# Kernel optimization log

Hardware: AMD Instinct MI355X
Metric: run time of the kernel (lower is better)

Reference implementation:

```python
import jax, jax.numpy as jnp
import numpy as np

HEADS = 16
ROPE_BASE = 10000.0


def _rope(x):
    # x: [b, h, n, d]. lucidrains partial rotary: RotaryEmbedding(head_dim//2)
    # rotates only the first rot_dim = d//2 channels, interleaved-pair style.
    d = x.shape[-1]
    rot = d // 2
    inv_freq = 1.0 / (ROPE_BASE ** (jnp.arange(0, rot, 2, dtype=jnp.float32) / rot))  # [rot//2]
    pos = jnp.arange(x.shape[2], dtype=jnp.float32)
    freqs = pos[:, None] * inv_freq[None, :]                  # [n, rot//2]
    cos, sin = jnp.cos(freqs), jnp.sin(freqs)
    xr, xp = x[..., :rot], x[..., rot:]
    x1, x2 = xr[..., 0::2], xr[..., 1::2]                     # interleaved pairs
    o1 = x1 * cos - x2 * sin
    o2 = x2 * cos + x1 * sin
    xr_out = jnp.stack([o1, o2], axis=-1).reshape(xr.shape)   # re-interleave
    return jnp.concatenate([xr_out, xp], axis=-1)


def setup_inputs() -> dict:
    key = jax.random.key(0)
    k0, k1 = jax.random.split(key)
    B, N, D = 2, 2048, 2048
    x = jax.random.normal(k0, (B, N, D), dtype=jnp.float32)
    W_qkv = jax.random.normal(k1, (3 * D, D), dtype=jnp.float32) * (D ** -0.5)
    b_qkv = jnp.zeros((3 * D,), dtype=jnp.float32)
    return {"x": x, "W_qkv": W_qkv, "b_qkv": b_qkv}


def reference(x, W_qkv, b_qkv):
    B, N, D = x.shape
    H = HEADS
    hd = D // H
    qkv = x @ W_qkv.T + b_qkv                                  # [b, n, 3d]
    q, k, v = jnp.split(qkv, 3, axis=-1)
    to_heads = lambda t: t.reshape(B, N, H, hd).transpose(0, 2, 1, 3)  # b h n d
    q, k, v = to_heads(q), to_heads(k), to_heads(v)
    q, k = _rope(q), _rope(k)
    scale = 1.0 / np.sqrt(hd)
    scores = jnp.einsum('bhnd,bhmd->bhnm', q, k) * scale
    causal = jnp.tril(jnp.ones((N, N), dtype=bool))
    scores = jnp.where(causal, scores, -jnp.inf)
    attn = jax.nn.softmax(scores, axis=-1)
    y = jnp.einsum('bhnm,bhmd->bhnd', attn, v)
    return y.transpose(0, 2, 1, 3).reshape(B, N, D)
```

## Files before the change

### kernel.cpp

```cpp
#include <hip/hip_runtime.h>
#include <hip/hip_bf16.h>
#include <math.h>

typedef unsigned short u16;
typedef unsigned int u32;
typedef __attribute__((ext_vector_type(8))) short bf16x8;
typedef __attribute__((ext_vector_type(4))) float f32x4;

#define B_ 2
#define N_ 2048
#define D_ 2048
#define H_ 16
#define HD 128
#define GK 2048

__device__ __forceinline__ u16 f2bf(float f) {
  u32 u = __float_as_uint(f);
  u = (u + 0x7fffu + ((u >> 16) & 1u)) >> 16;
  return (u16)u;
}

__device__ __forceinline__ u32 cvtpk(float lo, float hi) {
  u32 r;
  asm("v_cvt_pk_bf16_f32 %0, %1, %2" : "=v"(r) : "v"(lo), "v"(hi));
  return r;
}

__device__ __forceinline__ void gload_lds16(const void* g, void* l) {
  __builtin_amdgcn_global_load_lds(
      (const __attribute__((address_space(1))) u32*)g,
      (__attribute__((address_space(3))) u32*)l, 16, 0, 0);
}

__global__ __launch_bounds__(256) void cvt_kernel(const float* __restrict__ in,
                                                  u16* __restrict__ out, int n4) {
  int i = blockIdx.x * blockDim.x + threadIdx.x;
  int st = gridDim.x * blockDim.x;
  for (; i < n4; i += st) {
    float4 v = ((const float4*)in)[i];
    ushort4 o;
    o.x = f2bf(v.x); o.y = f2bf(v.y); o.z = f2bf(v.z); o.w = f2bf(v.w);
    ((ushort4*)out)[i] = o;
  }
}

__global__ __launch_bounds__(256) void rope_tbl_kernel(float* __restrict__ tbl) {
  int i = blockIdx.x * blockDim.x + threadIdx.x;
  if (i >= N_ * 32) return;
  int pos = i >> 5, p = i & 31;
  double inv = pow(10000.0, -(double)p / 32.0);
  double a = (double)pos * inv;
  tbl[2 * i]     = (float)cos(a);
  tbl[2 * i + 1] = (float)sin(a);
}

__global__ __launch_bounds__(512, 2) void qkv_gemm_kernel(
    const u16* __restrict__ X, const u16* __restrict__ W,
    const float* __restrict__ bias, const float* __restrict__ tbl,
    u16* __restrict__ Qo, u16* __restrict__ Ko, u16* __restrict__ Vo) {
  __shared__ char smem[114688];
  const int tid = threadIdx.x;
  const int lane = tid & 63;
  const int w = tid >> 6;
  const int wm = w >> 2, wn = w & 3;
  const int l15 = lane & 15, l4 = lane >> 4;

  const int bid = blockIdx.x;
  const int wg = (bid & 7) * 64 + (bid >> 3);
  const int n0 = (wg & 31) * 192;
  const int m0 = (wg >> 5) * 256;

  f32x4 acc[8][3];
#pragma unroll
  for (int fm = 0; fm < 8; ++fm)
#pragma unroll
    for (int fn = 0; fn < 3; ++fn)
#pragma unroll
      for (int q = 0; q < 4; ++q) acc[fm][fn][q] = 0.f;

  auto stageA = [&](int cb, int half, int k0) {
    char* dst = smem + cb * 57344 + half * 16384;
    const u16* src = X + (size_t)(m0 + half * 128) * GK + k0;
#pragma unroll
    for (int p = 0; p < 2; ++p) {
      int o = (w * 2 + p) * 1024 + lane * 16;
      int lo = o ^ (((o >> 7) & 7) << 4);
      gload_lds16(src + (size_t)(lo >> 7) * GK + ((lo & 127) >> 1),
                  dst + (w * 2 + p) * 1024);
    }
  };
  auto stageB = [&](int cb, int chunk, int k0) {
    char* dst = smem + cb * 57344 + 32768 + chunk * 8192;
    const u16* src = W + (size_t)(n0 + chunk * 64) * GK + k0;
    int o = w * 1024 + lane * 16;
    int lo = o ^ (((o >> 7) & 7) << 4);
    gload_lds16(src + (size_t)(lo >> 7) * GK + ((lo & 127) >> 1), dst + w * 1024);
  };

  const int NK = GK / 64;

  stageA(0, 0, 0); stageA(0, 1, 0);
  stageB(0, 0, 0); stageB(0, 1, 0); stageB(0, 2, 0);
  stageA(1, 0, 64); stageA(1, 1, 64);
  asm volatile("s_waitcnt vmcnt(4)" ::: "memory");
  __builtin_amdgcn_s_barrier();

  auto segment = [&](int T, int cb) {
    const char* Ab = smem + cb * 57344 + wm * 16384;
    const char* Bb = smem + cb * 57344 + 32768;
    const int kn1 = (T + 1) * 64, kn2 = (T + 2) * 64;
    bf16x8 a0[8], a1[8], b0[3], b1[3];

#pragma unroll
    for (int fm = 0; fm < 8; ++fm) {
      int r = fm * 16 + l15;
      a0[fm] = *(const bf16x8*)(Ab + ((r * 128 + l4 * 16) ^ ((r & 7) << 4)));
    }
#pragma unroll
    for (int fn = 0; fn < 3; ++fn) {
      int r = wn * 48 + fn * 16 + l15;
      b0[fn] = *(const bf16x8*)(Bb + ((r * 128 + l4 * 16) ^ ((r & 7) << 4)));
    }
    if (T + 1 < NK) { stageB(cb ^ 1, 0, kn1); stageB(cb ^ 1, 1, kn1); }
    __builtin_amdgcn_s_barrier();
    __builtin_amdgcn_s_setprio(1);
#pragma unroll
    for (int fm = 0; fm < 4; ++fm)
#pragma unroll
      for (int fn = 0; fn < 3; ++fn)
        acc[fm][fn] = __builtin_amdgcn_mfma_f32_16x16x32_bf16(a0[fm], b0[fn], acc[fm][fn], 0, 0, 0);
    __builtin_amdgcn_s_setprio(0);
    __builtin_amdgcn_s_barrier();

#pragma unroll
    for (int fm = 0; fm < 8; ++fm) {
      int r = fm * 16 + l15;
      a1[fm] = *(const bf16x8*)(Ab + ((r * 128 + 64 + l4 * 16) ^ ((r & 7) << 4)));
    }
#pragma unroll
    for (int fn = 0; fn < 3; ++fn) {
      int r = wn * 48 + fn * 16 + l15;
      b1[fn] = *(const bf16x8*)(Bb + ((r * 128 + 64 + l4 * 16) ^ ((r & 7) << 4)));
    }
    if (T + 1 < NK) stageB(cb ^ 1, 2, kn1);
    __builtin_amdgcn_s_barrier();
    __builtin_amdgcn_s_setprio(1);
#pragma unroll
    for (int fm = 4; fm < 8; ++fm)
#pragma unroll
      for (int fn = 0; fn < 3; ++fn)
        acc[fm][fn] = __builtin_amdgcn_mfma_f32_16x16x32_bf16(a0[fm], b0[fn], acc[fm][fn], 0, 0, 0);
    __builtin_amdgcn_s_setprio(0);
    __builtin_amdgcn_s_barrier();

    asm volatile("" ::: "memory");
    if (T + 2 < NK) stageA(cb, 0, kn2);
    __builtin_amdgcn_s_barrier();
    __builtin_amdgcn_s_setprio(1);
#pragma unroll
    for (int fm = 0; fm < 4; ++fm)
#pragma unroll
      for (int fn = 0; fn < 3; ++fn)
        acc[fm][fn] = __builtin_amdgcn_mfma_f32_16x16x32_bf16(a1[fm], b1[fn], acc[fm][fn], 0, 0, 0);
    __builtin_amdgcn_s_setprio(0);
    __builtin_amdgcn_s_barrier();

    asm volatile("" ::: "memory");
    if (T + 2 < NK) {
      stageA(cb, 1, kn2);
      asm volatile("s_waitcnt vmcnt(4)" ::: "memory");
    } else {
      asm volatile("s_waitcnt vmcnt(0)" ::: "memory");
    }
    __builtin_amdgcn_s_barrier();
    __builtin_amdgcn_s_setprio(1);
#pragma unroll
    for (int fm = 4; fm < 8; ++fm)
#pragma unroll
      for (int fn = 0; fn < 3; ++fn)
        acc[fm][fn] = __builtin_amdgcn_mfma_f32_16x16x32_bf16(a1[fm], b1[fn], acc[fm][fn], 0, 0, 0);
    __builtin_amdgcn_s_setprio(0);
    __builtin_amdgcn_s_barrier();
  };

  for (int T = 0; T < NK; T += 2) { segment(T, 0); segment(T + 1, 1); }

  const float QSCALE = 0.08838834764831845f;
#pragma unroll
  for (int fn = 0; fn < 3; ++fn) {
    int gn = n0 + wn * 48 + fn * 16 + l15;
    float bv = bias[gn];
    int sec = gn >> 11;
    int wi = gn & 2047;
    int h = wi >> 7;
    int d = wi & 127;
    u16* dstbase = (sec == 0) ? Qo : (sec == 1) ? Ko : Vo;
    float mulf = (sec == 0) ? QSCALE : 1.f;
    bool doRope = (sec < 2) && (d < 64);
    int pidx = d >> 1;
    bool odd = (d & 1) != 0;
#pragma unroll
    for (int fm = 0; fm < 8; ++fm) {
#pragma unroll
      for (int j = 0; j < 4; ++j) {
        int gm = m0 + wm * 128 + fm * 16 + l4 * 4 + j;
        int bb = gm >> 11;
        int pos = gm & 2047;
        float v = acc[fm][fn][j] + bv;
        float pr = __shfl_xor(v, 1);
        float ov = v;
        if (doRope) {
          float2 cs = ((const float2*)tbl)[pos * 32 + pidx];
          ov = odd ? (v * cs.x + pr * cs.y) : (v * cs.x - pr * cs.y);
        }
        dstbase[(size_t)((bb * H_ + h) * N_ + pos) * HD + d] = f2bf(ov * mulf);
      }
    }
  }
}

__global__ __launch_bounds__(256, 2) void flash_kernel(
    const u16* __restrict__ Q, const u16* __restrict__ K, const u16* __restrict__ V,
    float* __restrict__ Out) {
  __shared__ char smem[69632];

  const int tid = threadIdx.x, lane = tid & 63, w = tid >> 6;
  const int l15 = lane & 15, l4 = lane >> 4;

  const int bid = blockIdx.x;
  const int xcd = bid & 7, slot = bid >> 3;
  const int bh = xcd * 4 + (slot >> 4);
  const int x = 15 - (slot & 15);
  const int bb = bh >> 4, h = bh & 15;
  const size_t base = (size_t)bh * (N_ * HD);
  const int q0 = x * 128;
  const int nt = 2 * x + 2;

  bf16x8 qf[2][4];
#pragma unroll
  for (int g = 0; g < 2; ++g) {
    const u16* qp = Q + base + (size_t)(q0 + w * 32 + g * 16 + l15) * HD + l4 * 8;
#pragma unroll
    for (int kf = 0; kf < 4; ++kf) qf[g][kf] = *(const bf16x8*)(qp + kf * 32);
  }

  float m_r[2] = {-1e30f, -1e30f}, l_r[2] = {0.f, 0.f};
  f32x4 accO[2][8];
#pragma unroll
  for (int g = 0; g < 2; ++g)
#pragma unroll
    for (int df = 0; df < 8; ++df)
#pragma unroll
      for (int q = 0; q < 4; ++q) accO[g][df][q] = 0.f;

  auto stageK = [&](int buf, int t0) {
    const u16* kb = K + base + (size_t)t0 * HD;
    char* kt = smem + buf * 16384;
#pragma unroll
    for (int i = 0; i < 4; ++i) {
      int c = w * 4 + i;
      int o = c * 1024 + lane * 16;
      int lo = o ^ (((o >> 8) & 7) << 4);
      gload_lds16(kb + (lo >> 1), kt + c * 1024);
    }
  };
  auto loadV = [&](int t0, bf16x8* vr) {
    const u16* vp = V + base + (size_t)(t0 + lane) * HD + w * 32;
#pragma unroll
    for (int i = 0; i < 4; ++i) vr[i] = *(const bf16x8*)(vp + i * 8);
  };
  auto writeV = [&](int buf, const bf16x8* vr) {
    u16* vt = (u16*)(smem + 32768 + buf * 18432);
#pragma unroll
    for (int i = 0; i < 4; ++i)
#pragma unroll
      for (int jj = 0; jj < 8; ++jj)
        vt[(w * 32 + i * 8 + jj) * 72 + lane] = (u16)vr[i][jj];
  };

  const int src0 = l15 + 32 * (l4 & 1);
  const int src1 = src0 + 16;
  const int half = l4 >> 1;
  union U8 { u32 u[4]; bf16x8 v; };

  bf16x8 vreg[4];
  stageK(0, 0);
  loadV(0, vreg);
  writeV(0, vreg);
  __syncthreads();

  for (int t = 0; t < nt; ++t) {
    const int cur = t & 1;
    const int t0 = t * 64;
    const bool pre = (t + 1 < nt);
    if (pre) { stageK(cur ^ 1, t0 + 64); loadV(t0 + 64, vreg); }

    const char* kt = smem + cur * 16384;
    const u16* vt = (const u16*)(smem + 32768 + cur * 18432);

    f32x4 s[2][4];
#pragma unroll
    for (int cf = 0; cf < 4; ++cf) {
#pragma unroll
      for (int q = 0; q < 4; ++q) { s[0][cf][q] = 0.f; s[1][cf][q] = 0.f; }
      int row = cf * 16 + l15;
      int sw = (row & 7) << 4;
#pragma unroll
      for (int kf = 0; kf < 4; ++kf) {
        int off = (row * 256 + kf * 64 + l4 * 16) ^ sw;
        bf16x8 kfrag = *(const bf16x8*)(kt + off);
        s[0][cf] = __builtin_amdgcn_mfma_f32_16x16x32_bf16(kfrag, qf[0][kf], s[0][cf], 0, 0, 0);
        s[1][cf] = __builtin_amdgcn_mfma_f32_16x16x32_bf16(kfrag, qf[1][kf], s[1][cf], 0, 0, 0);
      }
    }

    u32 pk[2][4][2];
#pragma unroll
    for (int g = 0; g < 2; ++g) {
      const int qbase = q0 + w * 32 + g * 16;
      if (t0 + 63 > qbase) {
        const int qg = qbase + l15;
#pragma unroll
        for (int cf = 0; cf < 4; ++cf)
#pragma unroll
          for (int j = 0; j < 4; ++j) {
            int kvg = t0 + cf * 16 + l4 * 4 + j;
            if (kvg > qg) s[g][cf][j] = -1e30f;
          }
      }
      float pmax = s[g][0][0];
#pragma unroll
      for (int cf = 0; cf < 4; ++cf)
#pragma unroll
        for (int j = 0; j < 4; ++j) pmax = fmaxf(pmax, s[g][cf][j]);
      pmax = fmaxf(pmax, __shfl_xor(pmax, 16));
      pmax = fmaxf(pmax, __shfl_xor(pmax, 32));

      if (!__all(pmax <= m_r[g] + 8.f)) {
        float mn = fmaxf(m_r[g], pmax);
        float rs = __expf(m_r[g] - mn);
        m_r[g] = mn;
        l_r[g] *= rs;
#pragma unroll
        for (int df = 0; df < 8; ++df)
#pragma unroll
          for (int j = 0; j < 4; ++j) accO[g][df][j] *= rs;
      }

      float ps = 0.f;
#pragma unroll
      for (int cf = 0; cf < 4; ++cf) {
        float p0 = __expf(s[g][cf][0] - m_r[g]);
        float p1 = __expf(s[g][cf][1] - m_r[g]);
        float p2 = __expf(s[g][cf][2] - m_r[g]);
        float p3 = __expf(s[g][cf][3] - m_r[g]);
        ps += (p0 + p1) + (p2 + p3);
        pk[g][cf][0] = cvtpk(p0, p1);
        pk[g][cf][1] = cvtpk(p2, p3);
      }
      ps += __shfl_xor(ps, 16);
      ps += __shfl_xor(ps, 32);
      l_r[g] += ps;
    }

#pragma unroll
    for (int c = 0; c < 2; ++c) {
      const int c2 = 2 * c;
      U8 pu[2];
#pragma unroll
      for (int g = 0; g < 2; ++g) {
        u32 a0 = (u32)__shfl((int)pk[g][c2][0], src0);
        u32 b0 = (u32)__shfl((int)pk[g][c2 + 1][0], src0);
        u32 a1 = (u32)__shfl((int)pk[g][c2][1], src0);
        u32 b1 = (u32)__shfl((int)pk[g][c2 + 1][1], src0);
        u32 a2 = (u32)__shfl((int)pk[g][c2][0], src1);
        u32 b2 = (u32)__shfl((int)pk[g][c2 + 1][0], src1);
        u32 a3 = (u32)__shfl((int)pk[g][c2][1], src1);
        u32 b3 = (u32)__shfl((int)pk[g][c2 + 1][1], src1);
        pu[g].u[0] = half ? b0 : a0;
        pu[g].u[1] = half ? b1 : a1;
        pu[g].u[2] = half ? b2 : a2;
        pu[g].u[3] = half ? b3 : a3;
      }
#pragma unroll
      for (int df = 0; df < 8; ++df) {
        bf16x8 vf = *(const bf16x8*)(vt + (df * 16 + l15) * 72 + c * 32 + l4 * 8);
        accO[0][df] = __builtin_amdgcn_mfma_f32_16x16x32_bf16(vf, pu[0].v, accO[0][df], 0, 0, 0);
        accO[1][df] = __builtin_amdgcn_mfma_f32_16x16x32_bf16(vf, pu[1].v, accO[1][df], 0, 0, 0);
      }
    }

    if (pre) writeV(cur ^ 1, vreg);
    __syncthreads();
  }

  float* Obuf = (float*)(smem + w * 8448);
  const int l31 = lane & 31;
#pragma unroll
  for (int g = 0; g < 2; ++g) {
    float inv = 1.f / l_r[g];
#pragma unroll
    for (int df = 0; df < 8; ++df) {
      f32x4 v = accO[g][df];
#pragma unroll
      for (int j = 0; j < 4; ++j) v[j] *= inv;
      *(f32x4*)&Obuf[l15 * 132 + df * 16 + l4 * 4] = v;
    }
#pragma unroll
    for (int p = 0; p < 8; ++p) {
      int row = p * 2 + (lane >> 5);
      f32x4 v = *(const f32x4*)&Obuf[row * 132 + l31 * 4];
      int qg = q0 + w * 32 + g * 16 + row;
      *(f32x4*)&Out[(size_t)(bb * N_ + qg) * D_ + h * HD + l31 * 4] = v;
    }
  }
}

extern "C" void kernel_launch(void* const* d_in, const int* in_sizes, int n_in,
                              void* d_out, int out_size, void* d_ws, size_t ws_size,
                              hipStream_t stream) {
  const float* x  = (const float*)d_in[0];
  const float* Wq = (const float*)d_in[1];
  const float* bq = (const float*)d_in[2];
  float* out = (float*)d_out;
  char* ws = (char*)d_ws;

  u16* Qb  = (u16*)(ws);
  u16* Kb  = (u16*)(ws + 16777216);
  u16* Vb  = (u16*)(ws + 2 * 16777216);
  u16* Xb  = (u16*)(ws + 3 * 16777216);
  u16* Wb  = (u16*)(ws + 4 * 16777216);
  float* tbl = (float*)(ws + 4 * 16777216 + 25165824);

  cvt_kernel<<<2048, 256, 0, stream>>>(x, Xb, (B_ * N_ * D_) / 4);
  cvt_kernel<<<2048, 256, 0, stream>>>(Wq, Wb, (3 * D_ * D_) / 4);
  rope_tbl_kernel<<<(N_ * 32 + 255) / 256, 256, 0, stream>>>(tbl);
  qkv_gemm_kernel<<<512, 512, 0, stream>>>(Xb, Wb, bq, tbl, Qb, Kb, Vb);
  flash_kernel<<<512, 256, 0, stream>>>(Qb, Kb, Vb, out);
}
```

Before: 255.4 us.

## Triple-buffer A tiles and load fragments just-in-time in QKV GEMM

Restructures the QKV GEMM main loop so the A operand uses three LDS buffers and B uses two, with separate rotation. Each quarter-step now loads only the 4 A and 3 B fragments it needs, instead of preloading 8+8 A and 3+3 B, which cuts register pressure. Staging address arithmetic is hoisted out of the loop. LDS use grows from 112KB to 144KB, which may limit the 2-blocks-per-CU launch bound and changes where the LDS reads sit relative to the barriers.

```diff
diff --git a/kernel.cpp b/kernel.cpp
--- a/kernel.cpp
+++ b/kernel.cpp
@@ -58,7 +58,7 @@
     const u16* __restrict__ X, const u16* __restrict__ W,
     const float* __restrict__ bias, const float* __restrict__ tbl,
     u16* __restrict__ Qo, u16* __restrict__ Ko, u16* __restrict__ Vo) {
-  __shared__ char smem[114688];
+  __shared__ char smem[147456];
   const int tid = threadIdx.x;
   const int lane = tid & 63;
   const int w = tid >> 6;
@@ -70,6 +70,21 @@
   const int n0 = (wg & 31) * 192;
   const int m0 = (wg >> 5) * 256;
 
+  const int aof0 = (l4 * 16) ^ ((l15 & 7) << 4);
+  const int aof1 = (64 + l4 * 16) ^ ((l15 & 7) << 4);
+
+  int srowA[2], scolA[2];
+#pragma unroll
+  for (int p = 0; p < 2; ++p) {
+    int o = (w * 2 + p) * 1024 + lane * 16;
+    int lo = o ^ (((o >> 7) & 7) << 4);
+    srowA[p] = lo >> 7;
+    scolA[p] = (lo & 127) >> 1;
+  }
+  const int oB = w * 1024 + lane * 16;
+  const int loB = oB ^ (((oB >> 7) & 7) << 4);
+  const int srowB = loB >> 7, scolB = (loB & 127) >> 1;
+
   f32x4 acc[8][3];
 #pragma unroll
   for (int fm = 0; fm < 8; ++fm)
@@ -78,96 +93,92 @@
 #pragma unroll
       for (int q = 0; q < 4; ++q) acc[fm][fn][q] = 0.f;
 
-  auto stageA = [&](int cb, int half, int k0) {
-    char* dst = smem + cb * 57344 + half * 16384;
-    const u16* src = X + (size_t)(m0 + half * 128) * GK + k0;
+  auto stageA = [&](char* Abase, int half, int k0) {
 #pragma unroll
     for (int p = 0; p < 2; ++p) {
-      int o = (w * 2 + p) * 1024 + lane * 16;
-      int lo = o ^ (((o >> 7) & 7) << 4);
-      gload_lds16(src + (size_t)(lo >> 7) * GK + ((lo & 127) >> 1),
-                  dst + (w * 2 + p) * 1024);
+      gload_lds16(X + (size_t)(m0 + half * 128 + srowA[p]) * GK + k0 + scolA[p],
+                  Abase + half * 16384 + (w * 2 + p) * 1024);
     }
   };
-  auto stageB = [&](int cb, int chunk, int k0) {
-    char* dst = smem + cb * 57344 + 32768 + chunk * 8192;
-    const u16* src = W + (size_t)(n0 + chunk * 64) * GK + k0;
-    int o = w * 1024 + lane * 16;
-    int lo = o ^ (((o >> 7) & 7) << 4);
-    gload_lds16(src + (size_t)(lo >> 7) * GK + ((lo & 127) >> 1), dst + w * 1024);
+  auto stageB = [&](char* Bbase, int chunk, int k0) {
+    gload_lds16(W + (size_t)(n0 + chunk * 64 + srowB) * GK + k0 + scolB,
+                Bbase + chunk * 8192 + w * 1024);
   };
 
   const int NK = GK / 64;
 
-  stageA(0, 0, 0); stageA(0, 1, 0);
-  stageB(0, 0, 0); stageB(0, 1, 0); stageB(0, 2, 0);
-  stageA(1, 0, 64); stageA(1, 1, 64);
+  stageA(smem, 0, 0); stageA(smem, 1, 0);
+  stageB(smem + 98304, 0, 0); stageB(smem + 98304, 1, 0); stageB(smem + 98304, 2, 0);
+  stageA(smem + 32768, 0, 64); stageA(smem + 32768, 1, 64);
   asm volatile("s_waitcnt vmcnt(4)" ::: "memory");
   __builtin_amdgcn_s_barrier();
 
-  auto segment = [&](int T, int cb) {
-    const char* Ab = smem + cb * 57344 + wm * 16384;
-    const char* Bb = smem + cb * 57344 + 32768;
+  int at = 0;
+  for (int T = 0; T < NK; ++T) {
+    const int bt = T & 1;
+    int an2 = at + 2; if (an2 >= 3) an2 -= 3;
+    const char* Ab = smem + at * 32768 + wm * 16384;
+    const char* Bb = smem + 98304 + bt * 24576;
+    char* Bn = smem + 98304 + (bt ^ 1) * 24576;
+    char* An = smem + an2 * 32768;
     const int kn1 = (T + 1) * 64, kn2 = (T + 2) * 64;
-    bf16x8 a0[8], a1[8], b0[3], b1[3];
-
-#pragma unroll
-    for (int fm = 0; fm < 8; ++fm) {
-      int r = fm * 16 + l15;
-      a0[fm] = *(const bf16x8*)(Ab + ((r * 128 + l4 * 16) ^ ((r & 7) << 4)));
-    }
-#pragma unroll
-    for (int fn = 0; fn < 3; ++fn) {
-      int r = wn * 48 + fn * 16 + l15;
-      b0[fn] = *(const bf16x8*)(Bb + ((r * 128 + l4 * 16) ^ ((r & 7) << 4)));
-    }
-    if (T + 1 < NK) { stageB(cb ^ 1, 0, kn1); stageB(cb ^ 1, 1, kn1); }
+    const bool hasB = (T + 1 < NK), hasA = (T + 2 < NK);
+
+    bf16x8 b[3], a[4];
+
+#pragma unroll
+    for (int fn = 0; fn < 3; ++fn)
+      b[fn] = *(const bf16x8*)(Bb + (wn * 48 + fn * 16 + l15) * 128 + aof0);
+#pragma unroll
+    for (int fm = 0; fm < 4; ++fm)
+      a[fm] = *(const bf16x8*)(Ab + (fm * 16 + l15) * 128 + aof0);
+    if (hasB) { stageB(Bn, 0, kn1); stageB(Bn, 1, kn1); }
     __builtin_amdgcn_s_barrier();
     __builtin_amdgcn_s_setprio(1);
 #pragma unroll
     for (int fm = 0; fm < 4; ++fm)
 #pragma unroll
       for (int fn = 0; fn < 3; ++fn)
-        acc[fm][fn] = __builtin_amdgcn_mfma_f32_16x16x32_bf16(a0[fm], b0[fn], acc[fm][fn], 0, 0, 0);
+        acc[fm][fn] = __builtin_amdgcn_mfma_f32_16x16x32_bf16(a[fm], b[fn], acc[fm][fn], 0, 0, 0);
     __builtin_amdgcn_s_setprio(0);
     __builtin_amdgcn_s_barrier();
 
 #pragma unroll
-    for (int fm = 0; fm < 8; ++fm) {
-      int r = fm * 16 + l15;
-      a1[fm] = *(const bf16x8*)(Ab + ((r * 128 + 64 + l4 * 16) ^ ((r & 7) << 4)));
-    }
-#pragma unroll
-    for (int fn = 0; fn < 3; ++fn) {
-      int r = wn * 48 + fn * 16 + l15;
-      b1[fn] = *(const bf16x8*)(Bb + ((r * 128 + 64 + l4 * 16) ^ ((r & 7) << 4)));
-    }
-    if (T + 1 < NK) stageB(cb ^ 1, 2, kn1);
+    for (int fm = 0; fm < 4; ++fm)
+      a[fm] = *(const bf16x8*)(Ab + ((fm + 4) * 16 + l15) * 128 + aof0);
+    if (hasB) stageB(Bn, 2, kn1);
     __builtin_amdgcn_s_barrier();
     __builtin_amdgcn_s_setprio(1);
 #pragma unroll
-    for (int fm = 4; fm < 8; ++fm)
+    for (int fm = 0; fm < 4; ++fm)
 #pragma unroll
       for (int fn = 0; fn < 3; ++fn)
-        acc[fm][fn] = __builtin_amdgcn_mfma_f32_16x16x32_bf16(a0[fm], b0[fn], acc[fm][fn], 0, 0, 0);
+        acc[fm + 4][fn] = __builtin_amdgcn_mfma_f32_16x16x32_bf16(a[fm], b[fn], acc[fm + 4][fn], 0, 0, 0);
     __builtin_amdgcn_s_setprio(0);
     __builtin_amdgcn_s_barrier();
 
-    asm volatile("" ::: "memory");
-    if (T + 2 < NK) stageA(cb, 0, kn2);
+#pragma unroll
+    for (int fn = 0; fn < 3; ++fn)
+      b[fn] = *(const bf16x8*)(Bb + (wn * 48 + fn * 16 + l15) * 128 + aof1);
+#pragma unroll
+    for (int fm = 0; fm < 4; ++fm)
+      a[fm] = *(const bf16x8*)(Ab + (fm * 16 + l15) * 128 + aof1);
+    if (hasA) stageA(An, 0, kn2);
     __builtin_amdgcn_s_barrier();
     __builtin_amdgcn_s_setprio(1);
 #pragma unroll
     for (int fm = 0; fm < 4; ++fm)
 #pragma unroll
       for (int fn = 0; fn < 3; ++fn)
-        acc[fm][fn] = __builtin_amdgcn_mfma_f32_16x16x32_bf16(a1[fm], b1[fn], acc[fm][fn], 0, 0, 0);
+        acc[fm][fn] = __builtin_amdgcn_mfma_f32_16x16x32_bf16(a[fm], b[fn], acc[fm][fn], 0, 0, 0);
     __builtin_amdgcn_s_setprio(0);
     __builtin_amdgcn_s_barrier();
 
-    asm volatile("" ::: "memory");
-    if (T + 2 < NK) {
-      stageA(cb, 1, kn2);
+#pragma unroll
+    for (int fm = 0; fm < 4; ++fm)
+      a[fm] = *(const bf16x8*)(Ab + ((fm + 4) * 16 + l15) * 128 + aof1);
+    if (hasA) {
+      stageA(An, 1, kn2);
       asm volatile("s_waitcnt vmcnt(4)" ::: "memory");
     } else {
       asm volatile("s_waitcnt vmcnt(0)" ::: "memory");
@@ -175,15 +186,15 @@
     __builtin_amdgcn_s_barrier();
     __builtin_amdgcn_s_setprio(1);
 #pragma unroll
-    for (int fm = 4; fm < 8; ++fm)
+    for (int fm = 0; fm < 4; ++fm)
 #pragma unroll
       for (int fn = 0; fn < 3; ++fn)
-        acc[fm][fn] = __builtin_amdgcn_mfma_f32_16x16x32_bf16(a1[fm], b1[fn], acc[fm][fn], 0, 0, 0);
+        acc[fm + 4][fn] = __builtin_amdgcn_mfma_f32_16x16x32_bf16(a[fm], b[fn], acc[fm + 4][fn], 0, 0, 0);
     __builtin_amdgcn_s_setprio(0);
     __builtin_amdgcn_s_barrier();
-  };
-
-  for (int T = 0; T < NK; T += 2) { segment(T, 0); segment(T + 1, 1); }
+
+    at = (at + 1 == 3) ? 0 : at + 1;
+  }
 
   const float QSCALE = 0.08838834764831845f;
 #pragma unroll
```

Measured after the change: 254.5 us. No clear change (-0.4%).
